# Kernel tuning notes

Measured on AMD Instinct MI355X. Metric: run time of the kernel, lower is better.

The kernel has to match this reference:

```python
import jax, jax.numpy as jnp
import numpy as np
import math

NP, MNP, BS, DIM, NH, TOPK, FF = 512, 4096, 8, 256, 8, 32, 2048
HD = DIM // NH
EPS = 1e-5


def _ln(x, w, b):
    mu = jnp.mean(x, axis=-1, keepdims=True)
    var = jnp.mean((x - mu) ** 2, axis=-1, keepdims=True)
    return (x - mu) / jnp.sqrt(var + EPS) * w + b


def _lin(x, w, b):
    return x @ w.T + b


def setup_inputs() -> dict:
    key = jax.random.key(0)
    ks = jax.random.split(key, 16)
    s = 0.02
    d = {
        "tgt": jax.random.normal(ks[0], (NP, BS, DIM), jnp.float32),
        "memory": jax.random.normal(ks[1], (MNP, BS, DIM), jnp.float32),
        "query_pos": jax.random.normal(ks[2], (NP, BS, DIM), jnp.float32),
        "key_pos": jax.random.normal(ks[3], (MNP, BS, DIM), jnp.float32),
        "cw1": jax.random.normal(ks[4], (DIM, DIM), jnp.float32) * s,
        "cb1": jnp.zeros((DIM,), jnp.float32),
        "cw2": jax.random.normal(ks[5], (DIM, DIM), jnp.float32) * s,
        "cb2": jnp.zeros((DIM,), jnp.float32),
        "cw3": jax.random.normal(ks[6], (DIM, DIM), jnp.float32) * s,
        "cb3": jnp.zeros((DIM,), jnp.float32),
        "sa_in_w": jax.random.normal(ks[7], (3 * DIM, DIM), jnp.float32) * s,
        "sa_in_b": jnp.zeros((3 * DIM,), jnp.float32),
        "sa_out_w": jax.random.normal(ks[8], (DIM, DIM), jnp.float32) * s,
        "sa_out_b": jnp.zeros((DIM,), jnp.float32),
        "ln1_w": jnp.ones((DIM,), jnp.float32),
        "ln1_b": jnp.zeros((DIM,), jnp.float32),
        "ln2_w": jnp.ones((DIM,), jnp.float32),
        "ln2_b": jnp.zeros((DIM,), jnp.float32),
        "ln3_w": jnp.ones((DIM,), jnp.float32),
        "ln3_b": jnp.zeros((DIM,), jnp.float32),
        "ff1_w": jax.random.normal(ks[9], (FF, DIM), jnp.float32) * s,
        "ff1_b": jnp.zeros((FF,), jnp.float32),
        "ff2_w": jax.random.normal(ks[10], (DIM, FF), jnp.float32) * s,
        "ff2_b": jnp.zeros((DIM,), jnp.float32),
    }
    return d


def _forward(tgt, memory, query_pos, key_pos,
             cw1, cb1, cw2, cb2, cw3, cb3,
             sa_in_w, sa_in_b, sa_out_w, sa_out_b,
             ln1_w, ln1_b, ln2_w, ln2_b, ln3_w, ln3_b,
             ff1_w, ff1_b, ff2_w, ff2_b):
    npq, bs, dim = tgt.shape
    mnp = memory.shape[0]
    scale = 1.0 / math.sqrt(HD)

    # --- top-k cosine similarity neighbor selection (indices, non-diff) ---
    x = tgt.transpose(1, 0, 2)        # [bs, np, dim]
    m = memory.transpose(1, 0, 2)     # [bs, mnp, dim]
    xn = x / jnp.linalg.norm(x, axis=2, keepdims=True)
    mn = m / jnp.linalg.norm(m, axis=2, keepdims=True)
    sim = jnp.einsum('bnd,bmd->bnm', xn, mn)          # [bs, np, mnp]
    _, rns = jax.lax.top_k(sim, TOPK)                  # [bs, np, topk]

    # --- masked cross attention ---
    qc = (tgt + query_pos).transpose(1, 0, 2)          # [bs, np, dim]
    kc = (memory + key_pos).transpose(1, 0, 2)         # [bs, mnp, dim]
    vc = m
    qh = _lin(qc, cw1, cb1).reshape(bs, npq, NH, HD).transpose(0, 2, 1, 3)   # [bs,nh,np,hd]
    kh = _lin(kc, cw2, cb2).reshape(bs, mnp, NH, HD).transpose(0, 2, 1, 3)   # [bs,nh,mnp,hd]
    vh = _lin(vc, cw3, cb3).reshape(bs, mnp, NH, HD).transpose(0, 2, 1, 3)   # [bs,nh,mnp,hd]
    w = jnp.einsum('bhnd,bhmd->bhnm', qh, kh) * scale                         # [bs,nh,np,mnp]

    b_idx = jnp.arange(bs)[:, None, None]
    n_idx = jnp.arange(npq)[None, :, None]
    mask = jnp.zeros((bs, npq, mnp), w.dtype).at[b_idx, n_idx, rns].set(1.0)  # same for all heads
    mask = mask[:, None, :, :]                                                # [bs,1,np,mnp]
    w = w * mask + (-1e9) * (1.0 - mask)
    w = jax.nn.softmax(w, axis=3)
    cross = jnp.einsum('bhnm,bhmd->bhnd', w, vh).transpose(2, 0, 1, 3).reshape(npq, bs, dim)

    t = _ln(tgt + cross, ln1_w, ln1_b)

    # --- self attention (torch nn.MultiheadAttention, q=k=t+pos, v=t) ---
    wq, wk, wv = sa_in_w[:DIM], sa_in_w[DIM:2 * DIM], sa_in_w[2 * DIM:]
    bq, bk, bv = sa_in_b[:DIM], sa_in_b[DIM:2 * DIM], sa_in_b[2 * DIM:]
    qk = t + query_pos                                 # [np, bs, dim]
    q2 = _lin(qk, wq, bq).transpose(1, 0, 2).reshape(bs, npq, NH, HD).transpose(0, 2, 1, 3)
    k2 = _lin(qk, wk, bk).transpose(1, 0, 2).reshape(bs, npq, NH, HD).transpose(0, 2, 1, 3)
    v2 = _lin(t, wv, bv).transpose(1, 0, 2).reshape(bs, npq, NH, HD).transpose(0, 2, 1, 3)
    attn = jax.nn.softmax(jnp.einsum('bhnd,bhmd->bhnm', q2, k2) * scale, axis=-1)
    sa = jnp.einsum('bhnm,bhmd->bhnd', attn, v2).transpose(2, 0, 1, 3).reshape(npq, bs, dim)
    sa = _lin(sa, sa_out_w, sa_out_b)

    t = _ln(t + sa, ln2_w, ln2_b)

    # --- FFN (exact GELU, matching torch F.gelu default) ---
    ff = _lin(jax.nn.gelu(_lin(t, ff1_w, ff1_b), approximate=False), ff2_w, ff2_b)
    t = _ln(t + ff, ln3_w, ln3_b)
    return t


def reference(tgt, memory, query_pos, key_pos,
              cw1, cb1, cw2, cb2, cw3, cb3,
              sa_in_w, sa_in_b, sa_out_w, sa_out_b,
              ln1_w, ln1_b, ln2_w, ln2_b, ln3_w, ln3_b,
              ff1_w, ff1_b, ff2_w, ff2_b):
    return _forward(tgt, memory, query_pos, key_pos,
                    cw1, cb1, cw2, cb2, cw3, cb3,
                    sa_in_w, sa_in_b, sa_out_w, sa_out_b,
                    ln1_w, ln1_b, ln2_w, ln2_b, ln3_w, ln3_b,
                    ff1_w, ff1_b, ff2_w, ff2_b)
```

## Files before the change

### kernel.cpp

```cpp
#include <hip/hip_runtime.h>
#include <math.h>

typedef unsigned short u16;
typedef unsigned int u32;
typedef __bf16 bf16x8 __attribute__((ext_vector_type(8)));
typedef float f32x4 __attribute__((ext_vector_type(4)));

#define NPQ 512
#define MNP 4096
#define BSZ 8
#define DIM 256
#define NH 8
#define HD 32
#define TOPK 32
#define FFD 2048
#define SCALE 0.17677669529663687f

__device__ __forceinline__ u16 f2bf(float f){
  u32 u = __builtin_bit_cast(u32, f);
  u = (u + 0x7FFFu + ((u >> 16) & 1u)) >> 16;
  return (u16)u;
}
__device__ __forceinline__ float bf2f(u16 h){
  u32 u = ((u32)h) << 16;
  return __builtin_bit_cast(float, u);
}
__device__ __forceinline__ float wredsum(float v){
#pragma unroll
  for (int m = 32; m; m >>= 1) v += __shfl_xor(v, m, 64);
  return v;
}
__device__ __forceinline__ float gelu_exact(float x){
  return 0.5f * x * (1.0f + erff(x * 0.70710678118654752f));
}
__device__ __forceinline__ u32 keytr(u32 u){
  return u ^ (((u32)((int)u >> 31)) | 0x80000000u);
}

#define FP_MEM_B 32768
#define FP_TGT_B (32768 + 4096)
#define FP_TOT_B (32768 + 4096 + 5888)
__global__ __launch_bounds__(256)
void fused_prep(const float* __restrict__ mem, const float* __restrict__ kpos,
                u16* __restrict__ mnh, u16* __restrict__ mnl,
                u16* __restrict__ kc, u16* __restrict__ vc,
                const float* __restrict__ tgt, const float* __restrict__ qpos,
                u16* __restrict__ xnh, u16* __restrict__ xnl, u16* __restrict__ qc,
                const float* __restrict__ cb2, const float* __restrict__ cb3,
                float* __restrict__ cbKV,
                const float* __restrict__ s0, const float* __restrict__ s1,
                const float* __restrict__ s2, const float* __restrict__ s3,
                const float* __restrict__ s4, const float* __restrict__ s5,
                const float* __restrict__ s6, u16* __restrict__ wdst){
  __shared__ float sc[4];
  int gb = blockIdx.x, t = threadIdx.x;
  if (gb < FP_MEM_B){
    int r = gb;
    int b = r >> 12, mp = r & 4095;
    long src = ((long)mp*BSZ + b)*DIM + t;
    float x = mem[src];
    float s = wredsum(x*x);
    if ((t & 63) == 0) sc[t >> 6] = s;
    __syncthreads();
    float tot = sc[0]+sc[1]+sc[2]+sc[3];
    float xn = x / sqrtf(tot);
    u16 hi = f2bf(xn);
    long dst = (long)r*DIM + t;
    mnh[dst] = hi;
    mnl[dst] = f2bf(xn - bf2f(hi));
    kc[dst]  = f2bf(x + kpos[src]);
    vc[dst]  = f2bf(x);
  } else if (gb < FP_TGT_B){
    int r = gb - FP_MEM_B;
    if (r == 0){ cbKV[t] = cb2[t]; cbKV[256 + t] = cb3[t]; }
    int b = r >> 9, n = r & 511;
    long src = ((long)n*BSZ + b)*DIM + t;
    float x = tgt[src];
    float s = wredsum(x*x);
    if ((t & 63) == 0) sc[t >> 6] = s;
    __syncthreads();
    float tot = sc[0]+sc[1]+sc[2]+sc[3];
    float xn = x / sqrtf(tot);
    u16 hi = f2bf(xn);
    long dst = (long)r*DIM + t;
    xnh[dst] = hi;
    xnl[dst] = f2bf(xn - bf2f(hi));
    qc[dst]  = f2bf(x + qpos[src]);
  } else {
    int i = (gb - FP_TGT_B)*256 + t;
    if (i >= 1507328) return;
    const float* s; int base;
    if      (i <  65536){ s = s0; base = 0; }
    else if (i < 131072){ s = s1; base = 65536; }
    else if (i < 196608){ s = s2; base = 131072; }
    else if (i < 393216){ s = s3; base = 196608; }
    else if (i < 458752){ s = s4; base = 393216; }
    else if (i < 983040){ s = s5; base = 458752; }
    else                { s = s6; base = 983040; }
    wdst[i] = f2bf(s[i - base]);
  }
}

#define BST 136
__global__ __launch_bounds__(256, 2)
void sim_gemm(const u16* __restrict__ xnh, const u16* __restrict__ xnl,
              const u16* __restrict__ mnh, const u16* __restrict__ mnl,
              float* __restrict__ sim){
  __shared__ __align__(16) u16 Bh[128*BST];
  __shared__ __align__(16) u16 Bl[128*BST];
  int t = threadIdx.x, lane = t & 63, wv = t >> 6;
  int ml = lane & 15, quad = lane >> 4;
  int b = blockIdx.z;
  int tM = blockIdx.y * 128 + (wv & 1) * 64;
  int tN = blockIdx.x * 128;
  int nloc = (wv >> 1) * 64;
  const u16* Ah = xnh + ((long)b*NPQ + tM + ml)*DIM;
  const u16* Al = xnl + ((long)b*NPQ + tM + ml)*DIM;
  f32x4 acc[4][4];
  f32x4 zer = {0.f,0.f,0.f,0.f};
#pragma unroll
  for (int i = 0; i < 4; i++)
#pragma unroll
    for (int j = 0; j < 4; j++) acc[i][j] = zer;

  int srow = t >> 4, scg = t & 15;
  for (int half = 0; half < 2; half++){
    int k0 = half * 128;
    if (half) __syncthreads();
#pragma unroll
    for (int p = 0; p < 8; p++){
      int r = p*16 + srow;
      long g = ((long)b*MNP + tN + r)*DIM + k0 + scg*8;
      *(uint4*)(&Bh[r*BST + scg*8]) = *(const uint4*)(mnh + g);
      *(uint4*)(&Bl[r*BST + scg*8]) = *(const uint4*)(mnl + g);
    }
    bf16x8 ca[4], ca2[4], na[4], na2[4];
#pragma unroll
    for (int i = 0; i < 4; i++){
      ca[i]  = *(const bf16x8*)(Ah + (long)i*16*DIM + k0 + quad*8);
      ca2[i] = *(const bf16x8*)(Al + (long)i*16*DIM + k0 + quad*8);
    }
    __syncthreads();
#pragma unroll
    for (int kk = 0; kk < 128; kk += 32){
      if (kk < 96){
#pragma unroll
        for (int i = 0; i < 4; i++){
          na[i]  = *(const bf16x8*)(Ah + (long)i*16*DIM + k0 + kk + 32 + quad*8);
          na2[i] = *(const bf16x8*)(Al + (long)i*16*DIM + k0 + kk + 32 + quad*8);
        }
      }
      bf16x8 bh[4], bl[4];
#pragma unroll
      for (int j = 0; j < 4; j++){
        int nr = nloc + j*16 + ml;
        bh[j] = *(const bf16x8*)(&Bh[nr*BST + kk + quad*8]);
        bl[j] = *(const bf16x8*)(&Bl[nr*BST + kk + quad*8]);
      }
#pragma unroll
      for (int i = 0; i < 4; i++)
#pragma unroll
        for (int j = 0; j < 4; j++){
          acc[i][j] = __builtin_amdgcn_mfma_f32_16x16x32_bf16(ca[i],  bh[j], acc[i][j], 0, 0, 0);
          acc[i][j] = __builtin_amdgcn_mfma_f32_16x16x32_bf16(ca[i],  bl[j], acc[i][j], 0, 0, 0);
          acc[i][j] = __builtin_amdgcn_mfma_f32_16x16x32_bf16(ca2[i], bh[j], acc[i][j], 0, 0, 0);
        }
#pragma unroll
      for (int i = 0; i < 4; i++){ ca[i] = na[i]; ca2[i] = na2[i]; }
    }
  }
  long zC = (long)b * NPQ * MNP;
#pragma unroll
  for (int i = 0; i < 4; i++)
#pragma unroll
    for (int r = 0; r < 4; r++){
      int row = tM + i*16 + quad*4 + r;
#pragma unroll
      for (int j = 0; j < 4; j++){
        int col = tN + nloc + j*16 + ml;
        sim[zC + (long)row*MNP + col] = acc[i][j][r];
      }
    }
}

#define PBST 264
template<int KGROUPS, int OUT_BF16, int ACT>
__global__ __launch_bounds__(256)
void pgemm(const u16* __restrict__ A, const u16* __restrict__ A2, int selCol,
           const u16* __restrict__ B, const float* __restrict__ bias,
           void* __restrict__ Cv, int N){
  __shared__ __align__(16) u16 Bs[64*PBST];
  const int K = KGROUPS*256;
  int t = threadIdx.x, lane = t & 63, wv = t >> 6;
  int ml = lane & 15, quad = lane >> 4;
  int tM = blockIdx.x*64;
  int tN = blockIdx.y*64;
  const u16* Ab = (tN < selCol) ? A : A2;
  const u16* Arow = Ab + (long)(tM + wv*16 + ml)*K;
  f32x4 acc[4];
  f32x4 zer = {0.f,0.f,0.f,0.f};
#pragma unroll
  for (int nj = 0; nj < 4; nj++) acc[nj] = zer;
  int srow = t >> 5, scol = (t & 31)*8;
  for (int g = 0; g < KGROUPS; g++){
    if (g) __syncthreads();
#pragma unroll
    for (int p = 0; p < 8; p++){
      int r = p*8 + srow;
      *(uint4*)(&Bs[r*PBST + scol]) = *(const uint4*)(B + (long)(tN + r)*K + g*256 + scol);
    }
    bf16x8 a[8];
#pragma unroll
    for (int kk = 0; kk < 8; kk++)
      a[kk] = *(const bf16x8*)(Arow + g*256 + kk*32 + quad*8);
    __syncthreads();
#pragma unroll
    for (int kk = 0; kk < 8; kk++){
#pragma unroll
      for (int nj = 0; nj < 4; nj++){
        bf16x8 bv = *(const bf16x8*)(&Bs[(nj*16 + ml)*PBST + kk*32 + quad*8]);
        acc[nj] = __builtin_amdgcn_mfma_f32_16x16x32_bf16(a[kk], bv, acc[nj], 0, 0, 0);
      }
    }
  }
#pragma unroll
  for (int nj = 0; nj < 4; nj++){
    int col = tN + nj*16 + ml;
    float bv = bias[col];
#pragma unroll
    for (int r = 0; r < 4; r++){
      int row = tM + wv*16 + quad*4 + r;
      float v = acc[nj][r] + bv;
      if (ACT == 1) v = gelu_exact(v);
      long idx = (long)row * N + col;
      if (OUT_BF16) ((u16*)Cv)[idx] = f2bf(v);
      else ((float*)Cv)[idx] = v;
    }
  }
}

#define HSTRIDE 264
__global__ __launch_bounds__(256, 4)
void topk_k(const float* __restrict__ sim, int* __restrict__ rns){
  __shared__ int hist[4*HSTRIDE];
  __shared__ int sh_B, sh_above;
  __shared__ int scnt, stcnt;
  __shared__ int sties[256];
  int t = threadIdx.x, wv = t >> 6, lane = t & 63;
  long r = blockIdx.x;
  const uint4* row4 = (const uint4*)(sim + r*4096);
  u32 key[16];
#pragma unroll
  for (int j = 0; j < 4; j++){
    uint4 v = row4[j*256 + t];
    key[j*4+0] = keytr(v.x);
    key[j*4+1] = keytr(v.y);
    key[j*4+2] = keytr(v.z);
    key[j*4+3] = keytr(v.w);
  }
#pragma unroll
  for (int i = 0; i < 16; i++) asm volatile("" : "+v"(key[i]));
  if (t == 0){ scnt = 0; stcnt = 0; }
  u32 pref = 0;
  int k_above = 0;
#pragma unroll 1
  for (int round = 0; round < 4; round++){
    int shift = 24 - round*8;
    u32 pmask = (round == 0) ? 0u : (0xFFFFFFFFu << (shift + 8));
    for (int z = t; z < 4*HSTRIDE; z += 256) hist[z] = 0;
    __syncthreads();
    int* myh = hist + wv*HSTRIDE;
#pragma unroll 1
    for (int i = 0; i < 16; i++){
      bool pred = ((key[i] ^ pref) & pmask) == 0;
      u32 d = (key[i] >> shift) & 255;
      unsigned long long todo = __ballot(pred);
      while (todo){
        int src = (int)__builtin_ctzll(todo);
        u32 dd = __shfl(d, src, 64);
        unsigned long long match = __ballot(pred && d == dd);
        if (lane == src) atomicAdd(&myh[dd], (int)__popcll(match));
        todo &= ~match;
      }
    }
    __syncthreads();
    if (t < 64){
      int b0 = t*4+0, b1 = t*4+1, b2 = t*4+2, b3 = t*4+3;
      int h0 = hist[b0] + hist[HSTRIDE+b0] + hist[2*HSTRIDE+b0] + hist[3*HSTRIDE+b0];
      int h1 = hist[b1] + hist[HSTRIDE+b1] + hist[2*HSTRIDE+b1] + hist[3*HSTRIDE+b1];
      int h2 = hist[b2] + hist[HSTRIDE+b2] + hist[2*HSTRIDE+b2] + hist[3*HSTRIDE+b2];
      int h3 = hist[b3] + hist[HSTRIDE+b3] + hist[2*HSTRIDE+b3] + hist[3*HSTRIDE+b3];
      int local = h0 + h1 + h2 + h3;
      int s = local;
#pragma unroll
      for (int off = 1; off < 64; off <<= 1){
        int v = __shfl_down(s, off, 64);
        s += (t + off < 64) ? v : 0;
      }
      int excl = s - local;
      int a3 = excl, a2 = a3 + h3, a1 = a2 + h2, a0 = a1 + h1;
      int ka = k_above;
      if (ka + a3 < TOPK && ka + a3 + h3 >= TOPK){ sh_B = t*4+3; sh_above = ka + a3; }
      if (ka + a2 < TOPK && ka + a2 + h2 >= TOPK){ sh_B = t*4+2; sh_above = ka + a2; }
      if (ka + a1 < TOPK && ka + a1 + h1 >= TOPK){ sh_B = t*4+1; sh_above = ka + a1; }
      if (ka + a0 < TOPK && ka + a0 + h0 >= TOPK){ sh_B = t*4+0; sh_above = ka + a0; }
    }
    __syncthreads();
    pref |= ((u32)sh_B) << shift;
    k_above = sh_above;
  }
  int* out = rns + r*32;
#pragma unroll
  for (int i = 0; i < 16; i++){
    int gidx = (i >> 2)*1024 + t*4 + (i & 3);
    u32 kk = key[i];
    if (kk > pref){
      int p = atomicAdd(&scnt, 1);
      out[p] = gidx;
    } else if (kk == pref){
      int p = atomicAdd(&stcnt, 1);
      if (p < 256) sties[p] = gidx;
    }
  }
  __syncthreads();
  if (t == 0){
    int n = stcnt; if (n > 256) n = 256;
    int k_rem = TOPK - k_above;
    for (int s = 0; s < k_rem; s++){
      int mb = 0;
      for (int j = 1; j < n; j++) if (sties[j] < sties[mb]) mb = j;
      out[k_above + s] = sties[mb];
      sties[mb] = 0x7FFFFFFF;
    }
  }
}

#define CAS 272
__global__ __launch_bounds__(256)
void cross_attn(const u16* __restrict__ qh, const u16* __restrict__ khvh,
                const int* __restrict__ rns, float* __restrict__ crossO){
  __shared__ __align__(16) u16 Kg[32*CAS];
  __shared__ __align__(16) u16 Vg[32*CAS];
  __shared__ float qv[256];
  __shared__ int idxs[32];
  __shared__ float L[256];
  __shared__ float pm[8], ps[8];
  int r = blockIdx.x, t = threadIdx.x;
  int b = r >> 9;
  if (t < 32) idxs[t] = rns[(long)r*32 + t];
  qv[t] = bf2f(qh[(long)r*DIM + t]);
  __syncthreads();
  for (int i = t; i < 32*64; i += 256){
    int k = i >> 6, c = (i & 63) * 4;
    long src = ((long)b*MNP + idxs[k])*512 + c;
    *(ushort4*)(&Kg[k*CAS + c]) = *(const ushort4*)(khvh + src);
    *(ushort4*)(&Vg[k*CAS + c]) = *(const ushort4*)(khvh + src + 256);
  }
  __syncthreads();
  {
    int h = t >> 5, k = t & 31;
    float acc = 0.f;
#pragma unroll
    for (int d = 0; d < 32; d++) acc += qv[h*HD + d] * bf2f(Kg[k*CAS + h*HD + d]);
    L[t] = acc * SCALE;
  }
  __syncthreads();
  if (t < 8){
    float m = L[t*32];
    for (int k = 1; k < 32; k++) m = fmaxf(m, L[t*32 + k]);
    float s = 0.f;
    for (int k = 0; k < 32; k++) s += expf(L[t*32 + k] - m);
    pm[t] = m; ps[t] = s;
  }
  __syncthreads();
  {
    int h = t >> 5, dd = t & 31;
    float m = pm[h], inv = 1.0f/ps[h], acc = 0.f;
#pragma unroll
    for (int k = 0; k < 32; k++) acc += expf(L[h*32 + k] - m) * bf2f(Vg[k*CAS + h*HD + dd]);
    crossO[(long)r*DIM + t] = acc * inv;
  }
}

template<int MODE>
__global__ __launch_bounds__(256)
void ln_k(const float* __restrict__ xa, const float* __restrict__ xb,
          const float* __restrict__ qpos,
          const float* __restrict__ w, const float* __restrict__ bsh,
          float* __restrict__ yf, u16* __restrict__ yb, u16* __restrict__ qkb){
  __shared__ float sc[8];
  int r = blockIdx.x, t = threadIdx.x;
  int b = r >> 9, n = r & 511;
  long bidx = (long)r*DIM + t;
  long nidx = ((long)n*BSZ + b)*DIM + t;
  float x = (MODE == 1 ? xa[nidx] : xa[bidx]) + xb[bidx];
  float s  = wredsum(x);
  float s2 = wredsum(x*x);
  int wv = t >> 6;
  if ((t & 63) == 0){ sc[wv] = s; sc[4 + wv] = s2; }
  __syncthreads();
  float S  = sc[0]+sc[1]+sc[2]+sc[3];
  float S2 = sc[4]+sc[5]+sc[6]+sc[7];
  float mu  = S * (1.f/256.f);
  float var = S2 * (1.f/256.f) - mu*mu;
  float y = (x - mu) * (1.0f / sqrtf(var + 1e-5f)) * w[t] + bsh[t];
  if (MODE == 3){
    yf[nidx] = y;
  } else {
    yf[bidx] = y;
    yb[bidx] = f2bf(y);
    if (MODE == 1) qkb[bidx] = f2bf(y + qpos[nidx]);
  }
}

#define KST 40
#define PST 264
__global__ __launch_bounds__(256)
void self_attn(const u16* __restrict__ qkv, u16* __restrict__ sa_pre){
  __shared__ __align__(16) u16 KS[512*KST];
  __shared__ __align__(16) u16 QS[32*KST];
  __shared__ float mbuf[128];
  __shared__ float sbuf[128];
  u16* P  = KS;
  u16* Vt = KS + 32*PST;

  int qt = blockIdx.x, h = blockIdx.y, b = blockIdx.z;
  int t = threadIdx.x, lane = t & 63, wv = t >> 6;
  int ml = lane & 15, quad = lane >> 4;
  int n0 = qt * 32;

  {
    int q = t >> 3, d4 = (t & 7) * 4;
    const u16* src = qkv + ((long)b*NPQ + n0 + q)*768 + h*HD + d4;
    *(ushort2*)(QS + q*KST + d4)     = *(const ushort2*)(src);
    *(ushort2*)(QS + q*KST + d4 + 2) = *(const ushort2*)(src + 2);
  }
  for (int i = t; i < 512*8; i += 256){
    int j = i >> 3, d4 = (i & 7) * 4;
    const u16* src = qkv + ((long)b*NPQ + j)*768 + 256 + h*HD + d4;
    *(ushort2*)(KS + j*KST + d4)     = *(const ushort2*)(src);
    *(ushort2*)(KS + j*KST + d4 + 2) = *(const ushort2*)(src + 2);
  }
  __syncthreads();

  f32x4 acc[2][8];
  {
    bf16x8 aq[2];
#pragma unroll
    for (int mi = 0; mi < 2; mi++)
      aq[mi] = *(const bf16x8*)(QS + (mi*16 + ml)*KST + quad*8);
#pragma unroll
    for (int nj = 0; nj < 8; nj++){
      bf16x8 bk = *(const bf16x8*)(KS + (wv*128 + nj*16 + ml)*KST + quad*8);
      f32x4 z = {0.f,0.f,0.f,0.f};
#pragma unroll
      for (int mi = 0; mi < 2; mi++)
        acc[mi][nj] = __builtin_amdgcn_mfma_f32_16x16x32_bf16(aq[mi], bk, z, 0, 0, 0);
    }
  }
  float lmax[2][4];
#pragma unroll
  for (int mi = 0; mi < 2; mi++)
#pragma unroll
    for (int r = 0; r < 4; r++) lmax[mi][r] = -3.4e38f;
#pragma unroll
  for (int mi = 0; mi < 2; mi++)
#pragma unroll
    for (int nj = 0; nj < 8; nj++)
#pragma unroll
      for (int r = 0; r < 4; r++){
        float v = acc[mi][nj][r] * SCALE;
        acc[mi][nj][r] = v;
        lmax[mi][r] = fmaxf(lmax[mi][r], v);
      }
#pragma unroll
  for (int m = 1; m < 16; m <<= 1)
#pragma unroll
    for (int mi = 0; mi < 2; mi++)
#pragma unroll
      for (int r = 0; r < 4; r++)
        lmax[mi][r] = fmaxf(lmax[mi][r], __shfl_xor(lmax[mi][r], m, 64));
  if (ml == 0){
#pragma unroll
    for (int mi = 0; mi < 2; mi++)
#pragma unroll
      for (int r = 0; r < 4; r++)
        mbuf[(mi*16 + quad*4 + r)*4 + wv] = lmax[mi][r];
  }
  __syncthreads();
  float inv_[2][4];
  float lsum[2][4];
#pragma unroll
  for (int mi = 0; mi < 2; mi++)
#pragma unroll
    for (int r = 0; r < 4; r++){
      int row = mi*16 + quad*4 + r;
      float m0 = fmaxf(fmaxf(mbuf[row*4+0], mbuf[row*4+1]),
                       fmaxf(mbuf[row*4+2], mbuf[row*4+3]));
      float s = 0.f;
#pragma unroll
      for (int nj = 0; nj < 8; nj++){
        float e = __expf(acc[mi][nj][r] - m0);
        acc[mi][nj][r] = e;
        s += e;
      }
      lsum[mi][r] = s;
    }
#pragma unroll
  for (int m = 1; m < 16; m <<= 1)
#pragma unroll
    for (int mi = 0; mi < 2; mi++)
#pragma unroll
      for (int r = 0; r < 4; r++)
        lsum[mi][r] += __shfl_xor(lsum[mi][r], m, 64);
  if (ml == 0){
#pragma unroll
    for (int mi = 0; mi < 2; mi++)
#pragma unroll
      for (int r = 0; r < 4; r++)
        sbuf[(mi*16 + quad*4 + r)*4 + wv] = lsum[mi][r];
  }
  __syncthreads();
#pragma unroll
  for (int mi = 0; mi < 2; mi++)
#pragma unroll
    for (int r = 0; r < 4; r++){
      int row = mi*16 + quad*4 + r;
      inv_[mi][r] = 1.0f / (sbuf[row*4+0]+sbuf[row*4+1]+sbuf[row*4+2]+sbuf[row*4+3]);
    }

  int mi2 = wv >> 1, ni = wv & 1;
  f32x4 acc2 = {0.f,0.f,0.f,0.f};
  for (int half = 0; half < 2; half++){
    __syncthreads();
    if ((wv >> 1) == half){
      int cbase = (wv & 1) * 128;
#pragma unroll
      for (int mi = 0; mi < 2; mi++)
#pragma unroll
        for (int nj = 0; nj < 8; nj++)
#pragma unroll
          for (int r = 0; r < 4; r++)
            P[(mi*16 + quad*4 + r)*PST + cbase + nj*16 + ml] = f2bf(acc[mi][nj][r]);
    }
    for (int i = t; i < 2048; i += 256){
      int j = i >> 3, d4 = (i & 7) * 4;
      const u16* src = qkv + ((long)b*NPQ + half*256 + j)*768 + 512 + h*HD + d4;
      u16 v0 = src[0], v1 = src[1], v2e = src[2], v3 = src[3];
      Vt[(d4+0)*PST + j] = v0;
      Vt[(d4+1)*PST + j] = v1;
      Vt[(d4+2)*PST + j] = v2e;
      Vt[(d4+3)*PST + j] = v3;
    }
    __syncthreads();
#pragma unroll
    for (int k0 = 0; k0 < 256; k0 += 32){
      bf16x8 ap = *(const bf16x8*)(P  + (mi2*16 + ml)*PST + k0 + quad*8);
      bf16x8 bv = *(const bf16x8*)(Vt + (ni*16  + ml)*PST + k0 + quad*8);
      acc2 = __builtin_amdgcn_mfma_f32_16x16x32_bf16(ap, bv, acc2, 0, 0, 0);
    }
  }
#pragma unroll
  for (int r = 0; r < 4; r++){
    int row = mi2*16 + quad*4 + r;
    sa_pre[((long)b*NPQ + n0 + row)*DIM + h*HD + ni*16 + ml] =
        f2bf(acc2[r] * inv_[mi2][r]);
  }
}

extern "C" void kernel_launch(void* const* d_in, const int* in_sizes, int n_in,
                              void* d_out, int out_size, void* d_ws, size_t ws_size,
                              hipStream_t stream){
  (void)in_sizes; (void)n_in; (void)out_size; (void)ws_size;
  const float* tgt  = (const float*)d_in[0];
  const float* mem  = (const float*)d_in[1];
  const float* qpos = (const float*)d_in[2];
  const float* kpos = (const float*)d_in[3];
  const float* cw1  = (const float*)d_in[4];  const float* cb1 = (const float*)d_in[5];
  const float* cw2  = (const float*)d_in[6];  const float* cb2 = (const float*)d_in[7];
  const float* cw3  = (const float*)d_in[8];  const float* cb3 = (const float*)d_in[9];
  const float* saw  = (const float*)d_in[10]; const float* sab = (const float*)d_in[11];
  const float* sow  = (const float*)d_in[12]; const float* sob = (const float*)d_in[13];
  const float* ln1w = (const float*)d_in[14]; const float* ln1b = (const float*)d_in[15];
  const float* ln2w = (const float*)d_in[16]; const float* ln2b = (const float*)d_in[17];
  const float* ln3w = (const float*)d_in[18]; const float* ln3b = (const float*)d_in[19];
  const float* f1w  = (const float*)d_in[20]; const float* f1bs = (const float*)d_in[21];
  const float* f2w  = (const float*)d_in[22]; const float* f2bs = (const float*)d_in[23];

  char* base = (char*)d_ws;
  size_t off = 0;
  auto alloc = [&](size_t bytes) -> char* {
    char* p = base + off;
    off += (bytes + 255) & ~(size_t)255;
    return p;
  };
  u16* cw1b = (u16*)alloc(65536u*2);
  u16* cw2b = (u16*)alloc(65536u*2);
  u16* cw3b = (u16*)alloc(65536u*2);   (void)cw3b;
  u16* sawb = (u16*)alloc(196608u*2);
  u16* sowb = (u16*)alloc(65536u*2);
  u16* f1wb = (u16*)alloc(524288u*2);
  u16* f2wb = (u16*)alloc(524288u*2);
  int* rns  = (int*)alloc(4096u*32*4);
  float* cbKV = (float*)alloc(512*4);
  size_t offB = off;
  u16* xnh = (u16*)alloc((size_t)4096*256*2);
  u16* xnl = (u16*)alloc((size_t)4096*256*2);
  u16* mnh = (u16*)alloc((size_t)32768*256*2);
  u16* mnl = (u16*)alloc((size_t)32768*256*2);
  u16* qc  = (u16*)alloc((size_t)4096*256*2);
  u16* kc  = (u16*)alloc((size_t)32768*256*2);
  u16* vc  = (u16*)alloc((size_t)32768*256*2);
  float* sim = (float*)alloc((size_t)8*512*4096*4);

  char* regC = (char*)sim;
  u16* qh   = (u16*)regC;
  u16* khvh = (u16*)(regC + 2097152);
  char* regB = base + offB;
  size_t ob = 0;
  auto allocB = [&](size_t bytes) -> char* {
    char* p = regB + ob;
    ob += (bytes + 255) & ~(size_t)255;
    return p;
  };
  float* cross = (float*)allocB((size_t)4096*256*4);
  float* t1    = (float*)allocB((size_t)4096*256*4);
  u16*   t1b   = (u16*)allocB((size_t)4096*256*2);
  u16*   qkb   = (u16*)allocB((size_t)4096*256*2);
  u16*   qkv   = (u16*)allocB((size_t)4096*768*2);
  u16*   sa_pre= (u16*)allocB((size_t)4096*256*2);
  float* sa    = (float*)allocB((size_t)4096*256*4);
  float* t2    = (float*)allocB((size_t)4096*256*4);
  u16*   t2b   = (u16*)allocB((size_t)4096*256*2);
  u16*   h1    = (u16*)allocB((size_t)4096*2048*2);
  float* ff    = (float*)allocB((size_t)4096*256*4);

  const int BIG = 1 << 30;
  dim3 blk(256);
  fused_prep<<<dim3(FP_TOT_B), blk, 0, stream>>>(
      mem, kpos, mnh, mnl, kc, vc,
      tgt, qpos, xnh, xnl, qc, cb2, cb3, cbKV,
      cw1, cw2, cw3, saw, sow, f1w, f2w, cw1b);
  sim_gemm<<<dim3(32,4,8), blk, 0, stream>>>(xnh, xnl, mnh, mnl, sim);
  topk_k<<<dim3(4096), blk, 0, stream>>>(sim, rns);
  pgemm<1,1,0><<<dim3(64,4), blk, 0, stream>>>(qc, qc, BIG, cw1b, cb1, qh, 256);
  pgemm<1,1,0><<<dim3(512,8), blk, 0, stream>>>(kc, vc, 256, cw2b, cbKV, khvh, 512);
  cross_attn<<<dim3(4096), blk, 0, stream>>>(qh, khvh, rns, cross);
  ln_k<1><<<dim3(4096), blk, 0, stream>>>(tgt, cross, qpos, ln1w, ln1b, t1, t1b, qkb);
  pgemm<1,1,0><<<dim3(64,12), blk, 0, stream>>>(qkb, t1b, 512, sawb, sab, qkv, 768);
  self_attn<<<dim3(16,8,8), blk, 0, stream>>>(qkv, sa_pre);
  pgemm<1,0,0><<<dim3(64,4), blk, 0, stream>>>(sa_pre, sa_pre, BIG, sowb, sob, sa, 256);
  ln_k<2><<<dim3(4096), blk, 0, stream>>>(t1, sa, nullptr, ln2w, ln2b, t2, t2b, nullptr);
  pgemm<1,1,1><<<dim3(64,32), blk, 0, stream>>>(t2b, t2b, BIG, f1wb, f1bs, h1, 2048);
  pgemm<8,0,0><<<dim3(64,4), blk, 0, stream>>>(h1, h1, BIG, f2wb, f2bs, ff, 256);
  ln_k<3><<<dim3(4096), blk, 0, stream>>>(t2, ff, nullptr, ln3w, ln3b, (float*)d_out, nullptr, nullptr);
}
```

Measured before the change: 458.8 us.

## Restructure top-k radix select into 12/8/8/4-bit rounds with direct LDS atomics

Replaces the four 8-bit radix rounds, which used ballot/shuffle warp aggregation into per-wave histograms, with a templated radix round. The new split is 12, 8, 8 and 4 bits, and each key does a plain shared-memory atomicAdd into one block-wide histogram. The scan now covers up to 4096 bins using a per-wave prefix and a cross-wave sum. This is meant to cut the serialized ballot loop cost and to make the 4096-key candidate set shrink faster after the first round. In exchange, contention on the shared histogram rises and the first round uses a 16KB histogram, which may hurt occupancy.

```diff
diff --git a/kernel.cpp b/kernel.cpp
--- a/kernel.cpp
+++ b/kernel.cpp
@@ -239,14 +239,65 @@
   }
 }
 
-#define HSTRIDE 264
+template<int SHIFT, int NB, int FIRST>
+__device__ __forceinline__
+void radix_round(const u32* key, u32& pref, int& k_above,
+                 int* hist, int* wsum, int* sel){
+  constexpr int LOG  = (NB == 4096) ? 12 : (NB == 256) ? 8 : 4;
+  constexpr int NBPT = (NB > 256) ? (NB / 256) : 1;
+  constexpr int OWN  = (NB < 256) ? NB : 256;
+  constexpr u32 pmask = FIRST ? 0u : (u32)(0xFFFFFFFFull << (SHIFT + LOG));
+  int t = threadIdx.x, lane = t & 63, wv = t >> 6;
+  for (int z = t; z < NB; z += 256) hist[z] = 0;
+  if (t < 4) wsum[t] = 0;
+  __syncthreads();
+#pragma unroll
+  for (int i = 0; i < 16; i++){
+    if (((key[i] ^ pref) & pmask) == 0)
+      atomicAdd(&hist[(key[i] >> SHIFT) & (NB - 1)], 1);
+  }
+  __syncthreads();
+  int local = 0, s = 0;
+  if (t < OWN){
+#pragma unroll
+    for (int j = 0; j < NBPT; j++) local += hist[t*NBPT + j];
+    s = local;
+#pragma unroll
+    for (int off = 1; off < 64; off <<= 1){
+      int v = __shfl_down(s, off, 64);
+      s += (lane + off < 64 && t + off < OWN) ? v : 0;
+    }
+    if (lane == 0) wsum[wv] = s;
+  }
+  __syncthreads();
+  if (t < OWN){
+    int cross = 0;
+#pragma unroll
+    for (int w = 1; w < 4; w++) if (w > wv) cross += wsum[w];
+    int runs = (s - local) + cross;
+    int ka = k_above;
+#pragma unroll
+    for (int j = NBPT - 1; j >= 0; j--){
+      int hj = hist[t*NBPT + j];
+      if (ka + runs < TOPK && ka + runs + hj >= TOPK){
+        sel[0] = t*NBPT + j; sel[1] = ka + runs;
+      }
+      runs += hj;
+    }
+  }
+  __syncthreads();
+  pref |= ((u32)sel[0]) << SHIFT;
+  k_above = sel[1];
+}
+
 __global__ __launch_bounds__(256, 4)
 void topk_k(const float* __restrict__ sim, int* __restrict__ rns){
-  __shared__ int hist[4*HSTRIDE];
-  __shared__ int sh_B, sh_above;
-  __shared__ int scnt, stcnt;
+  __shared__ int hist[4096];
   __shared__ int sties[256];
-  int t = threadIdx.x, wv = t >> 6, lane = t & 63;
+  __shared__ int wsum[4];
+  __shared__ int sel2[2];
+  __shared__ int cnt2[2];
+  int t = threadIdx.x;
   long r = blockIdx.x;
   const uint4* row4 = (const uint4*)(sim + r*4096);
   u32 key[16];
@@ -260,71 +311,29 @@
   }
 #pragma unroll
   for (int i = 0; i < 16; i++) asm volatile("" : "+v"(key[i]));
-  if (t == 0){ scnt = 0; stcnt = 0; }
+  if (t == 0){ cnt2[0] = 0; cnt2[1] = 0; }
   u32 pref = 0;
   int k_above = 0;
-#pragma unroll 1
-  for (int round = 0; round < 4; round++){
-    int shift = 24 - round*8;
-    u32 pmask = (round == 0) ? 0u : (0xFFFFFFFFu << (shift + 8));
-    for (int z = t; z < 4*HSTRIDE; z += 256) hist[z] = 0;
-    __syncthreads();
-    int* myh = hist + wv*HSTRIDE;
-#pragma unroll 1
-    for (int i = 0; i < 16; i++){
-      bool pred = ((key[i] ^ pref) & pmask) == 0;
-      u32 d = (key[i] >> shift) & 255;
-      unsigned long long todo = __ballot(pred);
-      while (todo){
-        int src = (int)__builtin_ctzll(todo);
-        u32 dd = __shfl(d, src, 64);
-        unsigned long long match = __ballot(pred && d == dd);
-        if (lane == src) atomicAdd(&myh[dd], (int)__popcll(match));
-        todo &= ~match;
-      }
-    }
-    __syncthreads();
-    if (t < 64){
-      int b0 = t*4+0, b1 = t*4+1, b2 = t*4+2, b3 = t*4+3;
-      int h0 = hist[b0] + hist[HSTRIDE+b0] + hist[2*HSTRIDE+b0] + hist[3*HSTRIDE+b0];
-      int h1 = hist[b1] + hist[HSTRIDE+b1] + hist[2*HSTRIDE+b1] + hist[3*HSTRIDE+b1];
-      int h2 = hist[b2] + hist[HSTRIDE+b2] + hist[2*HSTRIDE+b2] + hist[3*HSTRIDE+b2];
-      int h3 = hist[b3] + hist[HSTRIDE+b3] + hist[2*HSTRIDE+b3] + hist[3*HSTRIDE+b3];
-      int local = h0 + h1 + h2 + h3;
-      int s = local;
-#pragma unroll
-      for (int off = 1; off < 64; off <<= 1){
-        int v = __shfl_down(s, off, 64);
-        s += (t + off < 64) ? v : 0;
-      }
-      int excl = s - local;
-      int a3 = excl, a2 = a3 + h3, a1 = a2 + h2, a0 = a1 + h1;
-      int ka = k_above;
-      if (ka + a3 < TOPK && ka + a3 + h3 >= TOPK){ sh_B = t*4+3; sh_above = ka + a3; }
-      if (ka + a2 < TOPK && ka + a2 + h2 >= TOPK){ sh_B = t*4+2; sh_above = ka + a2; }
-      if (ka + a1 < TOPK && ka + a1 + h1 >= TOPK){ sh_B = t*4+1; sh_above = ka + a1; }
-      if (ka + a0 < TOPK && ka + a0 + h0 >= TOPK){ sh_B = t*4+0; sh_above = ka + a0; }
-    }
-    __syncthreads();
-    pref |= ((u32)sh_B) << shift;
-    k_above = sh_above;
-  }
+  radix_round<20, 4096, 1>(key, pref, k_above, hist, wsum, sel2);
+  radix_round<12,  256, 0>(key, pref, k_above, hist, wsum, sel2);
+  radix_round< 4,  256, 0>(key, pref, k_above, hist, wsum, sel2);
+  radix_round< 0,   16, 0>(key, pref, k_above, hist, wsum, sel2);
   int* out = rns + r*32;
 #pragma unroll
   for (int i = 0; i < 16; i++){
     int gidx = (i >> 2)*1024 + t*4 + (i & 3);
     u32 kk = key[i];
     if (kk > pref){
-      int p = atomicAdd(&scnt, 1);
+      int p = atomicAdd(&cnt2[0], 1);
       out[p] = gidx;
     } else if (kk == pref){
-      int p = atomicAdd(&stcnt, 1);
+      int p = atomicAdd(&cnt2[1], 1);
       if (p < 256) sties[p] = gidx;
     }
   }
   __syncthreads();
   if (t == 0){
-    int n = stcnt; if (n > 256) n = 256;
+    int n = cnt2[1]; if (n > 256) n = 256;
     int k_rem = TOPK - k_above;
     for (int s = 0; s < k_rem; s++){
       int mb = 0;
```

Result: faster. 429.3 us (-6.4%).
